# Performance work log

Measured on AMD Instinct MI355X. Metric: run time of the kernel, lower is better.

## Reference

```python
import jax, jax.numpy as jnp
import numpy as np

F_NODE, F_BOND, D, LAYERS = 133, 14, 256, 3
N_NODE, N_BOND, N_NB = 100000, 200000, 600000


def hardswish(x):
    return x * jnp.clip(x + 3.0, 0.0, 6.0) * (1.0 / 6.0)


def setup_inputs() -> dict:
    key = jax.random.key(0)
    ks = jax.random.split(key, 16)

    def xav(k, fan_in, fan_out):
        std = (2.0 / (fan_in + fan_out)) ** 0.5
        return (jax.random.normal(k, (fan_in, fan_out), jnp.float32) * std)

    inp = {
        "node": jax.random.normal(ks[0], (N_NODE, F_NODE), jnp.float32),
        "bond": jax.random.normal(ks[1], (N_BOND, F_BOND), jnp.float32),
        "connect": jax.random.randint(ks[2], (3, N_BOND), 0, N_NODE, jnp.int32),
        "bond_neighbour": jax.random.randint(ks[3], (2, N_NB), 0, N_BOND, jnp.int32),
        # learned parameters, stored as [in, out] (torch Linear transposed)
        "w_node": xav(ks[4], F_NODE, D), "b_node": jnp.zeros((D,), jnp.float32),
        "w_node_final": xav(ks[5], F_NODE + D, D), "b_node_final": jnp.zeros((D,), jnp.float32),
        "w_bond": xav(ks[6], F_NODE + F_BOND, D), "b_bond": jnp.zeros((D,), jnp.float32),
        "w_bond_final": xav(ks[7], F_NODE + F_BOND + D, D), "b_bond_final": jnp.zeros((D,), jnp.float32),
        "w_z": xav(ks[8], F_NODE + F_BOND + D, D), "b_z": jnp.zeros((D,), jnp.float32),
        "w_r": xav(ks[9], F_NODE + F_BOND + D, D), "b_r": jnp.zeros((D,), jnp.float32),
        "u": xav(ks[10], D, D),
        "w_m": xav(ks[11], F_NODE + F_BOND, D), "b_m": jnp.zeros((D,), jnp.float32),
        "w_n": xav(ks[12], F_NODE, D), "b_n": jnp.zeros((D,), jnp.float32),
        "u_n": xav(ks[13], 2 * D, D),
    }
    return inp


def reference(node, bond, connect, bond_neighbour,
              w_node, b_node, w_node_final, b_node_final,
              w_bond, b_bond, w_bond_final, b_bond_final,
              w_z, b_z, w_r, b_r, u, w_m, b_m, w_n, b_n, u_n):
    i_idx, j_idx = connect[0], connect[1]          # [E]; connect[2] (reverse) unused
    ij_idx, ki_idx = bond_neighbour[0], bond_neighbour[1]  # [E_nb]

    init_bond = jnp.concatenate([node[i_idx], bond], axis=-1)  # [E, f_node+f_bond]
    init_node = node                                           # [N, f_node]

    mess_bond = hardswish(init_bond @ w_bond + b_bond)  # [E, D]
    mess_node = hardswish(node @ w_node + b_node)       # [N, D]

    for _ in range(LAYERS):
        mess_ki = mess_bond[ki_idx]                                   # [E_nb, D]
        s_ij = jax.ops.segment_sum(mess_ki, ij_idx, num_segments=N_BOND)
        z_ij = jax.nn.sigmoid(jnp.concatenate([init_bond, s_ij], -1) @ w_z + b_z)
        r_ki = jax.nn.sigmoid(jnp.concatenate([init_bond[ij_idx], mess_ki], -1) @ w_r + b_r)
        r_ij = jax.ops.segment_sum(r_ki * mess_ki, ij_idx, num_segments=N_BOND)
        m_ij = jnp.tanh(init_bond @ w_m + b_m + r_ij @ u)
        mess_bond = (1.0 - z_ij) * s_ij + z_ij * m_ij                 # [E, D]
        aggr_node = jax.ops.segment_sum(mess_bond, j_idx, num_segments=N_NODE)
        mess_node = hardswish(init_node @ w_n + b_n
                              + jnp.concatenate([mess_node, aggr_node], -1) @ u_n)

    mess_bond = hardswish(jnp.concatenate([init_bond, mess_bond], -1) @ w_bond_final + b_bond_final)
    mess_node = hardswish(jnp.concatenate([init_node, mess_node], -1) @ w_node_final + b_node_final)
    # dropout is identity in eval mode
    return mess_node, mess_bond
```

## Files before the change

### kernel.cpp

```cpp
#include <hip/hip_runtime.h>
#include <hip/hip_bf16.h>

#define NN 100000
#define NE 200000
#define NB 600000
#define FN 133
#define FB 14
#define FIB 147
#define DD 256
#define NEPAD (196 * 1024)
#define NNPAD (98 * 1024)

typedef __hip_bfloat16 bf16;
typedef __attribute__((ext_vector_type(8))) short short8;
typedef __attribute__((ext_vector_type(4))) float f32x4;

__device__ __forceinline__ float hswish(float x) {
    float c = fminf(fmaxf(x + 3.f, 0.f), 6.f);
    return x * c * (1.f / 6.f);
}
__device__ __forceinline__ float sigmoidf(float x) {
    return 1.f / (1.f + __expf(-x));
}
__device__ __forceinline__ float tanh_fast(float x) {
    return 1.f - 2.f / (1.f + __expf(2.f * x));
}
__device__ __forceinline__ float bf2f(unsigned short u) {
    union { unsigned int i; float f; } c; c.i = (unsigned int)u << 16; return c.f;
}
__device__ __forceinline__ unsigned short f2bf(float v) {
    bf16 b = __float2bfloat16(v);
    unsigned short u; __builtin_memcpy(&u, &b, 2); return u;
}
__device__ __forceinline__ void unp8(short8 v, float* f) {
    #pragma unroll
    for (int j = 0; j < 8; j++) {
        short s = v[j]; unsigned short u; __builtin_memcpy(&u, &s, 2);
        f[j] = bf2f(u);
    }
}
__device__ __forceinline__ uint4 pk8(const float* f) {
    uint4 v;
    v.x = f2bf(f[0]) | ((unsigned)f2bf(f[1]) << 16);
    v.y = f2bf(f[2]) | ((unsigned)f2bf(f[3]) << 16);
    v.z = f2bf(f[4]) | ((unsigned)f2bf(f[5]) << 16);
    v.w = f2bf(f[6]) | ((unsigned)f2bf(f[7]) << 16);
    return v;
}

__global__ __launch_bounds__(256) void fill_kernel(float* __restrict__ p, float v, long n4) {
    long i = (long)blockIdx.x * 256 + threadIdx.x;
    long st = (long)gridDim.x * 256;
    float4 z = {v, v, v, v};
    for (; i < n4; i += st) ((float4*)p)[i] = z;
}

__global__ __launch_bounds__(256) void build_ib_bf(
    const float* __restrict__ node, const float* __restrict__ bond,
    const int* __restrict__ i_idx, bf16* __restrict__ IB)
{
    int t = blockIdx.x * 256 + threadIdx.x;
    int row = t >> 6;
    if (row >= NE) return;
    int lane = t & 63;
    if (lane >= 40) return;
    int src = i_idx[row];
    int c = lane * 4;
    unsigned short us[4];
    #pragma unroll
    for (int j = 0; j < 4; j++) {
        int k = c + j;
        float v = 0.f;
        if (k < FN)       v = node[(size_t)src * FN + k];
        else if (k < FIB) v = bond[(size_t)row * FB + (k - FN)];
        us[j] = f2bf(v);
    }
    ushort4 o = {us[0], us[1], us[2], us[3]};
    *(ushort4*)((unsigned short*)IB + (size_t)row * 160 + c) = o;
}

__global__ __launch_bounds__(256) void zero2_kernel(int* __restrict__ offE, int* __restrict__ offN)
{
    int i = blockIdx.x * 256 + threadIdx.x;
    if (i < NEPAD) offE[i] = 0;
    else if (i < NEPAD + NNPAD) offN[i - NEPAD] = 0;
}

__global__ __launch_bounds__(256) void count2_kernel(
    const int* __restrict__ ij, const int* __restrict__ jidx,
    int* __restrict__ offE, int* __restrict__ offN)
{
    int i = blockIdx.x * 256 + threadIdx.x;
    if (i < NB) atomicAdd(&offE[ij[i]], 1);
    else if (i < NB + NE) atomicAdd(&offN[jidx[i - NB]], 1);
}

__global__ __launch_bounds__(256) void scan_block2(
    int* __restrict__ offE, int* __restrict__ offN,
    int* __restrict__ bsumE, int* __restrict__ bsumN)
{
    __shared__ int lds[256];
    int* data; int* bs; int bb;
    if ((int)blockIdx.x < 196) { data = offE; bs = bsumE; bb = blockIdx.x; }
    else                       { data = offN; bs = bsumN; bb = blockIdx.x - 196; }
    int base = bb * 1024 + threadIdx.x * 4;
    int c0 = data[base], c1 = data[base + 1], c2 = data[base + 2], c3 = data[base + 3];
    int t = c0 + c1 + c2 + c3;
    lds[threadIdx.x] = t;
    __syncthreads();
    int x = t;
    for (int off = 1; off < 256; off <<= 1) {
        int y = (threadIdx.x >= off) ? lds[threadIdx.x - off] : 0;
        __syncthreads();
        x += y; lds[threadIdx.x] = x;
        __syncthreads();
    }
    int excl = x - t;
    data[base] = excl; data[base + 1] = excl + c0;
    data[base + 2] = excl + c0 + c1; data[base + 3] = excl + c0 + c1 + c2;
    if (threadIdx.x == 255) bs[bb] = x;
}

__global__ __launch_bounds__(256) void scan_bsum2(int* __restrict__ bsumE, int* __restrict__ bsumN)
{
    __shared__ int lds[256];
    int* bs = blockIdx.x ? bsumN : bsumE;
    int n = blockIdx.x ? 98 : 196;
    int t = (threadIdx.x < n) ? bs[threadIdx.x] : 0;
    lds[threadIdx.x] = t;
    __syncthreads();
    int x = t;
    for (int off = 1; off < 256; off <<= 1) {
        int y = (threadIdx.x >= off) ? lds[threadIdx.x - off] : 0;
        __syncthreads();
        x += y; lds[threadIdx.x] = x;
        __syncthreads();
    }
    if (threadIdx.x < n) bs[threadIdx.x] = x - t;
}

__global__ __launch_bounds__(256) void scan_add_copy2(
    int* __restrict__ offE, int* __restrict__ offN,
    const int* __restrict__ bsumE, const int* __restrict__ bsumN,
    int* __restrict__ curE, int* __restrict__ curN)
{
    int i = blockIdx.x * 256 + threadIdx.x;
    if (i < NEPAD) {
        int v = offE[i] + bsumE[i >> 10];
        offE[i] = v; curE[i] = v;
    } else if (i < NEPAD + NNPAD) {
        int j = i - NEPAD;
        int v = offN[j] + bsumN[j >> 10];
        offN[j] = v; curN[j] = v;
    }
}

__global__ __launch_bounds__(256) void lists2_kernel(
    const int* __restrict__ ij, const int* __restrict__ ki, const int* __restrict__ jidx,
    int* __restrict__ curE, int* __restrict__ curN,
    int* __restrict__ nbLst, int* __restrict__ agLst)
{
    int i = blockIdx.x * 256 + threadIdx.x;
    if (i < NB) { int p = atomicAdd(&curE[ij[i]], 1); nbLst[p] = ki[i]; }
    else if (i < NB + NE) {
        int e = i - NB;
        int p = atomicAdd(&curN[jidx[e]], 1); agLst[p] = e;
    }
}

__global__ __launch_bounds__(256) void pack_all(
    const float* __restrict__ w_r, const float* __restrict__ w_z,
    const float* __restrict__ w_bond, const float* __restrict__ w_m,
    const float* __restrict__ w_node, const float* __restrict__ w_n,
    const float* __restrict__ u_, const float* __restrict__ u_n,
    const float* __restrict__ w_bf, const float* __restrict__ w_nf,
    bf16* __restrict__ wt)
{
    int idx = blockIdx.x * 256 + threadIdx.x;
    if (idx >= 786432) return;
    float v = 0.f;
    if (idx < 245760) {
        int r = idx / 40960;
        int loc = idx - r * 40960;
        int n = loc / 160, k = loc % 160;
        const float* W = (r == 0) ? w_r : (r == 1) ? w_z : (r == 2) ? w_bond
                       : (r == 3) ? w_m : (r == 4) ? w_node : w_n;
        int K1 = (r < 4) ? FIB : FN;
        if (k < K1) v = W[(size_t)k * DD + n];
    } else if (idx < 442368) {
        int r = (idx - 245760) / 65536;
        int loc = (idx - 245760) - r * 65536;
        int n = loc / 256, k = loc % 256;
        const float* W = (r == 0) ? (w_r + (size_t)FIB * DD)
                       : (r == 1) ? (w_z + (size_t)FIB * DD) : u_;
        v = W[(size_t)k * DD + n];
    } else if (idx < 573440) {
        int loc = idx - 442368;
        int n = loc / 512, k = loc % 512;
        v = u_n[(size_t)k * DD + n];
    } else {
        int r = (idx - 573440) / 106496;
        int loc = (idx - 573440) - r * 106496;
        int n = loc / 416, k = loc % 416;
        const float* W = r ? w_nf : w_bf;
        int K1 = r ? FN : FIB;
        if (k < K1)        v = W[(size_t)k * DD + n];
        else if (k >= 160) v = W[(size_t)(K1 + k - 160) * DD + n];
    }
    wt[idx] = __float2bfloat16(v);
}

__global__ __launch_bounds__(256) void seg_sr_kernel(
    const bf16* __restrict__ MB, const bf16* __restrict__ TR,
    const bf16* __restrict__ PR, const int* __restrict__ off,
    const int* __restrict__ lst,
    bf16* __restrict__ S, bf16* __restrict__ R)
{
    int sid = blockIdx.x * 4 + (threadIdx.x >> 6);
    if (sid >= NE) return;
    int lane = threadIdx.x & 63;
    ushort4 up = *(const ushort4*)((const unsigned short*)PR + (size_t)sid * DD + lane * 4);
    float p0 = bf2f(up.x), p1 = bf2f(up.y), p2 = bf2f(up.z), p3 = bf2f(up.w);
    int b = off[sid], e = off[sid + 1];
    float s0 = 0, s1 = 0, s2 = 0, s3 = 0;
    float r0 = 0, r1 = 0, r2 = 0, r3 = 0;
    for (int t = b; t < e; t++) {
        int src = lst[t];
        ushort4 um = *(const ushort4*)((const unsigned short*)MB + (size_t)src * DD + lane * 4);
        ushort4 ut = *(const ushort4*)((const unsigned short*)TR + (size_t)src * DD + lane * 4);
        float m0 = bf2f(um.x), m1 = bf2f(um.y), m2 = bf2f(um.z), m3 = bf2f(um.w);
        s0 += m0; s1 += m1; s2 += m2; s3 += m3;
        r0 += sigmoidf(p0 + bf2f(ut.x)) * m0;
        r1 += sigmoidf(p1 + bf2f(ut.y)) * m1;
        r2 += sigmoidf(p2 + bf2f(ut.z)) * m2;
        r3 += sigmoidf(p3 + bf2f(ut.w)) * m3;
    }
    ushort4 os = {f2bf(s0), f2bf(s1), f2bf(s2), f2bf(s3)};
    ushort4 orr = {f2bf(r0), f2bf(r1), f2bf(r2), f2bf(r3)};
    *(ushort4*)((unsigned short*)S + (size_t)sid * DD + lane * 4) = os;
    *(ushort4*)((unsigned short*)R + (size_t)sid * DD + lane * 4) = orr;
}

__global__ __launch_bounds__(512) void blend2(
    const bf16* __restrict__ S, const bf16* __restrict__ R,
    const bf16* __restrict__ WTz2, const bf16* __restrict__ WTu,
    const bf16* __restrict__ PZ, const bf16* __restrict__ PM,
    bf16* __restrict__ MB)
{
    __shared__ __align__(16) unsigned short As[128 * 72];
    __shared__ __align__(16) unsigned short Bs[128 * 72];
    const int tid = threadIdx.x;
    const int row0 = blockIdx.x * 128, col0 = blockIdx.y * 128;
    const int lane = tid & 63, w = tid >> 6;
    const int wr = w >> 1, wc = w & 1;
    const int fr = lane & 15, ko = (lane >> 4) * 8;

    f32x4 acc1[2][4] = {};
    f32x4 acc2[2][4] = {};

    #pragma unroll
    for (int ph = 0; ph < 2; ph++) {
        const bf16* A = (ph == 0) ? S : R;
        const bf16* W = (ph == 0) ? WTz2 : WTu;
        for (int k0 = 0; k0 < DD; k0 += 64) {
            {
                int mloc = tid >> 2, kq = (tid & 3) * 16;
                int mg = row0 + mloc;
                uint4 va = {0, 0, 0, 0}, va2 = {0, 0, 0, 0};
                if (mg < NE) {
                    va  = *(const uint4*)((const unsigned short*)A + (size_t)mg * DD + k0 + kq);
                    va2 = *(const uint4*)((const unsigned short*)A + (size_t)mg * DD + k0 + kq + 8);
                }
                uint4 vb  = *(const uint4*)((const unsigned short*)W + (size_t)(col0 + mloc) * DD + k0 + kq);
                uint4 vb2 = *(const uint4*)((const unsigned short*)W + (size_t)(col0 + mloc) * DD + k0 + kq + 8);
                *(uint4*)&As[mloc * 72 + kq] = va;
                *(uint4*)&As[mloc * 72 + kq + 8] = va2;
                *(uint4*)&Bs[mloc * 72 + kq] = vb;
                *(uint4*)&Bs[mloc * 72 + kq + 8] = vb2;
            }
            __syncthreads();
            #pragma unroll
            for (int kk = 0; kk < 64; kk += 32) {
                short8 af[2], bf8[4];
                #pragma unroll
                for (int mf = 0; mf < 2; mf++)
                    af[mf] = *(const short8*)&As[(wr * 32 + mf * 16 + fr) * 72 + kk + ko];
                #pragma unroll
                for (int nf = 0; nf < 4; nf++)
                    bf8[nf] = *(const short8*)&Bs[(wc * 64 + nf * 16 + fr) * 72 + kk + ko];
                #pragma unroll
                for (int mf = 0; mf < 2; mf++)
                    #pragma unroll
                    for (int nf = 0; nf < 4; nf++) {
                        if (ph == 0)
                            acc1[mf][nf] = __builtin_amdgcn_mfma_f32_16x16x32_bf16(af[mf], bf8[nf], acc1[mf][nf], 0, 0, 0);
                        else
                            acc2[mf][nf] = __builtin_amdgcn_mfma_f32_16x16x32_bf16(af[mf], bf8[nf], acc2[mf][nf], 0, 0, 0);
                    }
            }
            __syncthreads();
        }
    }

    #pragma unroll
    for (int mf = 0; mf < 2; mf++) {
        #pragma unroll
        for (int i = 0; i < 4; i++) {
            int mloc = wr * 32 + mf * 16 + (lane >> 4) * 4 + i;
            int gm = row0 + mloc;
            if (gm >= NE) continue;
            #pragma unroll
            for (int nf = 0; nf < 4; nf++) {
                int gc = col0 + wc * 64 + nf * 16 + fr;
                size_t idx = (size_t)gm * DD + gc;
                float z  = sigmoidf(acc1[mf][nf][i] + __bfloat162float(PZ[idx]));
                float mm = tanh_fast(acc2[mf][nf][i] + __bfloat162float(PM[idx]));
                float s  = __bfloat162float(S[idx]);
                MB[idx] = __float2bfloat16((1.f - z) * s + z * mm);
            }
        }
    }
}

__global__ __launch_bounds__(512) void pairk(
    int trblocks,
    const bf16* __restrict__ MBn, const bf16* __restrict__ WTr2,
    bf16* __restrict__ TRo,
    const bf16* __restrict__ MN, const int* __restrict__ offN,
    const int* __restrict__ agLst, const bf16* __restrict__ WTnu,
    const bf16* __restrict__ PN, bf16* __restrict__ MNout)
{
    __shared__ __align__(16) unsigned short As[128 * 40];
    __shared__ __align__(16) unsigned short Bs[256 * 40];
    const int tid = threadIdx.x, lane = tid & 63, w = tid >> 6;
    const int fr = lane & 15, ko = (lane >> 4) * 8;
    const int mloc = tid >> 2, kq = (tid & 3) * 8;

    if ((int)blockIdx.x < trblocks) {
        const int row0 = blockIdx.x * 128;
        const int wr = w >> 2, wc = w & 3;
        const int mg = row0 + mloc;
        f32x4 acc[4][4] = {};
        for (int k0 = 0; k0 < 256; k0 += 32) {
            uint4 v = {0, 0, 0, 0};
            if (mg < NE)
                v = *(const uint4*)((const unsigned short*)MBn + (size_t)mg * DD + k0 + kq);
            *(uint4*)&As[mloc * 40 + kq] = v;
            #pragma unroll
            for (int it = 0; it < 2; ++it) {
                int nloc = (tid >> 2) + it * 128;
                *(uint4*)&Bs[nloc * 40 + kq] =
                    *(const uint4*)((const unsigned short*)WTr2 + (size_t)nloc * DD + k0 + kq);
            }
            __syncthreads();
            short8 af[4], bw[4];
            #pragma unroll
            for (int mf = 0; mf < 4; mf++)
                af[mf] = *(const short8*)&As[(wr * 64 + mf * 16 + fr) * 40 + ko];
            #pragma unroll
            for (int nf = 0; nf < 4; nf++)
                bw[nf] = *(const short8*)&Bs[(wc * 64 + nf * 16 + fr) * 40 + ko];
            #pragma unroll
            for (int mf = 0; mf < 4; mf++)
                #pragma unroll
                for (int nf = 0; nf < 4; nf++)
                    acc[mf][nf] = __builtin_amdgcn_mfma_f32_16x16x32_bf16(af[mf], bw[nf], acc[mf][nf], 0, 0, 0);
            __syncthreads();
        }
        #pragma unroll
        for (int mf = 0; mf < 4; mf++)
            #pragma unroll
            for (int i = 0; i < 4; i++) {
                int ml = wr * 64 + mf * 16 + (lane >> 4) * 4 + i;
                int gm = row0 + ml;
                if (gm >= NE) continue;
                #pragma unroll
                for (int nf = 0; nf < 4; nf++) {
                    int gc = wc * 64 + nf * 16 + fr;
                    TRo[(size_t)gm * DD + gc] = __float2bfloat16(acc[mf][nf][i]);
                }
            }
    } else {
        const int bx = blockIdx.x - trblocks;
        const int row0 = bx * 128;
        const int wr = w >> 2, wc = w & 3;
        const int mg = row0 + mloc;
        int eb = 0, ee = 0;
        if (mg < NN) { eb = offN[mg]; ee = offN[mg + 1]; }
        f32x4 acc[4][4] = {};
        for (int k0 = 0; k0 < 512; k0 += 32) {
            const int kg = k0 + kq;
            uint4 v = {0, 0, 0, 0};
            if (mg < NN) {
                if (kg < 256) {
                    v = *(const uint4*)((const unsigned short*)MN + (size_t)mg * DD + kg);
                } else {
                    const int kk = kg - 256;
                    float a[8] = {0, 0, 0, 0, 0, 0, 0, 0};
                    for (int t = eb; t < ee; t++) {
                        int src = agLst[t];
                        float m8[8];
                        unp8(*(const short8*)((const unsigned short*)MBn + (size_t)src * DD + kk), m8);
                        #pragma unroll
                        for (int j = 0; j < 8; j++) a[j] += m8[j];
                    }
                    v = pk8(a);
                }
            }
            *(uint4*)&As[mloc * 40 + kq] = v;
            #pragma unroll
            for (int it = 0; it < 2; ++it) {
                int nloc = (tid >> 2) + it * 128;
                *(uint4*)&Bs[nloc * 40 + kq] =
                    *(const uint4*)((const unsigned short*)WTnu + (size_t)nloc * 512 + k0 + kq);
            }
            __syncthreads();
            short8 af[4], bw[4];
            #pragma unroll
            for (int mf = 0; mf < 4; mf++)
                af[mf] = *(const short8*)&As[(wr * 64 + mf * 16 + fr) * 40 + ko];
            #pragma unroll
            for (int nf = 0; nf < 4; nf++)
                bw[nf] = *(const short8*)&Bs[(wc * 64 + nf * 16 + fr) * 40 + ko];
            #pragma unroll
            for (int mf = 0; mf < 4; mf++)
                #pragma unroll
                for (int nf = 0; nf < 4; nf++)
                    acc[mf][nf] = __builtin_amdgcn_mfma_f32_16x16x32_bf16(af[mf], bw[nf], acc[mf][nf], 0, 0, 0);
            __syncthreads();
        }
        #pragma unroll
        for (int mf = 0; mf < 4; mf++)
            #pragma unroll
            for (int i = 0; i < 4; i++) {
                int ml = wr * 64 + mf * 16 + (lane >> 4) * 4 + i;
                int gm = row0 + ml;
                if (gm >= NN) continue;
                #pragma unroll
                for (int nf = 0; nf < 4; nf++) {
                    int gc = wc * 64 + nf * 16 + fr;
                    size_t idx = (size_t)gm * DD + gc;
                    MNout[idx] = __float2bfloat16(
                        hswish(acc[mf][nf][i] + __bfloat162float(PN[idx])));
                }
            }
    }
}

template <int BN, int NT, int DUAL, int EPB>
__device__ __forceinline__ void bg_body(
    const void* __restrict__ A1, int a1stride, int a1kw, int a1real, int a1f32,
    const void* __restrict__ A2, int a2stride, int a2kw, int a2real, int a2f32,
    const bf16* __restrict__ WT1, const bf16* __restrict__ WT2, int KT,
    const float* __restrict__ bias1, const float* __restrict__ bias2,
    void* __restrict__ out1, void* __restrict__ out2, int M,
    int row0, int col0,
    unsigned short* As, unsigned short* Bs, unsigned short* Bs2)
{
    constexpr int BM = 128;
    constexpr int nWc = BN / 64;
    constexpr int nWr = (NT / 64) / nWc;
    constexpr int MSPAN = BM / nWr;
    constexpr int MFR = MSPAN / 16;
    const int tid = threadIdx.x;
    const int lane = tid & 63, w = tid >> 6;
    const int wr = w / nWc, wc = w % nWc;
    const int fr = lane & 15, ko = (lane >> 4) * 8;

    f32x4 acc[MFR][4] = {};
    f32x4 acc2[DUAL ? MFR : 1][DUAL ? 4 : 1] = {};

    for (int k0 = 0; k0 < KT; k0 += 32) {
        #pragma unroll
        for (int it = 0; it < BM * 4 / NT; ++it) {
            int mloc = (tid >> 2) + it * (NT / 4);
            int mg = row0 + mloc;
            bool mok = (mg < M);
            int kq = (tid & 3) * 8;
            int kg = k0 + kq;
            const void* p; int stride, real, isf; int kk;
            if (kg < a1kw) { p = A1; stride = a1stride; real = a1real; isf = a1f32; kk = kg; }
            else           { p = A2; stride = a2stride; real = a2real; isf = a2f32; kk = kg - a1kw; }
            uint4 v = {0, 0, 0, 0};
            if (mok) {
                if (!isf) {
                    v = *(const uint4*)((const bf16*)p + (size_t)mg * stride + kk);
                } else {
                    const float* fp = (const float*)p + (size_t)mg * stride;
                    unsigned short us[8];
                    #pragma unroll
                    for (int j = 0; j < 8; j++)
                        us[j] = (kk + j < real) ? f2bf(fp[kk + j]) : (unsigned short)0;
                    v.x = us[0] | ((unsigned)us[1] << 16);
                    v.y = us[2] | ((unsigned)us[3] << 16);
                    v.z = us[4] | ((unsigned)us[5] << 16);
                    v.w = us[6] | ((unsigned)us[7] << 16);
                }
            }
            *(uint4*)&As[mloc * 40 + kq] = v;
        }
        #pragma unroll
        for (int it = 0; it < BN * 4 / NT; ++it) {
            int nloc = (tid >> 2) + it * (NT / 4);
            int kq = (tid & 3) * 8;
            *(uint4*)&Bs[nloc * 40 + kq] =
                *(const uint4*)&WT1[(size_t)(col0 + nloc) * KT + k0 + kq];
            if (DUAL)
                *(uint4*)&Bs2[nloc * 40 + kq] =
                    *(const uint4*)&WT2[(size_t)(col0 + nloc) * KT + k0 + kq];
        }
        __syncthreads();
        short8 a1f[MFR], b1f[4], b2f[DUAL ? 4 : 1];
        #pragma unroll
        for (int mf = 0; mf < MFR; mf++)
            a1f[mf] = *(const short8*)&As[(wr * MSPAN + mf * 16 + fr) * 40 + ko];
        #pragma unroll
        for (int nf = 0; nf < 4; nf++) {
            b1f[nf] = *(const short8*)&Bs[(wc * 64 + nf * 16 + fr) * 40 + ko];
            if (DUAL)
                b2f[nf] = *(const short8*)&Bs2[(wc * 64 + nf * 16 + fr) * 40 + ko];
        }
        #pragma unroll
        for (int mf = 0; mf < MFR; mf++)
            #pragma unroll
            for (int nf = 0; nf < 4; nf++) {
                acc[mf][nf] = __builtin_amdgcn_mfma_f32_16x16x32_bf16(a1f[mf], b1f[nf], acc[mf][nf], 0, 0, 0);
                if (DUAL)
                    acc2[mf][nf] = __builtin_amdgcn_mfma_f32_16x16x32_bf16(a1f[mf], b2f[nf], acc2[mf][nf], 0, 0, 0);
            }
        __syncthreads();
    }

    #pragma unroll
    for (int mf = 0; mf < MFR; mf++) {
        #pragma unroll
        for (int i = 0; i < 4; i++) {
            int mloc = wr * MSPAN + mf * 16 + (lane >> 4) * 4 + i;
            int gm = row0 + mloc;
            if (gm >= M) continue;
            #pragma unroll
            for (int nf = 0; nf < 4; nf++) {
                int gc = col0 + wc * 64 + nf * 16 + fr;
                size_t idx = (size_t)gm * DD + gc;
                float v = acc[mf][nf][i];
                if (EPB == 0) {
                    if (bias1) v += bias1[gc];
                    ((bf16*)out1)[idx] = __float2bfloat16(v);
                } else if (EPB == 2) {
                    ((bf16*)out1)[idx] = __float2bfloat16(hswish(v + bias1[gc]));
                    ((bf16*)out2)[idx] = __float2bfloat16(acc2[mf][nf][i] + bias2[gc]);
                } else if (EPB == 3) {
                    ((bf16*)out1)[idx] = __float2bfloat16(v + bias1[gc]);
                    ((bf16*)out2)[idx] = __float2bfloat16(acc2[mf][nf][i] + bias2[gc]);
                } else {
                    ((float*)out1)[idx] = hswish(v + bias1[gc]);
                }
            }
        }
    }
}

__device__ __forceinline__ void bg64_body(
    const void* __restrict__ A1, int a1stride, int a1kw, int a1real, int a1f32,
    const void* __restrict__ A2, int a2stride, int a2kw, int a2real, int a2f32,
    const bf16* __restrict__ WT1, int KT, const float* __restrict__ bias1,
    float* __restrict__ out1, int M, int row0,
    unsigned short* As, unsigned short* Bs)
{
    const int tid = threadIdx.x;
    const int lane = tid & 63, w = tid >> 6;
    const int wr = w >> 2, wc = w & 3;
    const int fr = lane & 15, ko = (lane >> 4) * 8;

    f32x4 acc[2][4] = {};

    for (int k0 = 0; k0 < KT; k0 += 32) {
        if (tid < 256) {
            int mloc = tid >> 2, kq = (tid & 3) * 8;
            int mg = row0 + mloc;
            int kg = k0 + kq;
            const void* p; int stride, real, isf; int kk;
            if (kg < a1kw) { p = A1; stride = a1stride; real = a1real; isf = a1f32; kk = kg; }
            else           { p = A2; stride = a2stride; real = a2real; isf = a2f32; kk = kg - a1kw; }
            uint4 v = {0, 0, 0, 0};
            if (mg < M) {
                if (!isf) {
                    v = *(const uint4*)((const bf16*)p + (size_t)mg * stride + kk);
                } else {
                    const float* fp = (const float*)p + (size_t)mg * stride;
                    unsigned short us[8];
                    #pragma unroll
                    for (int j = 0; j < 8; j++)
                        us[j] = (kk + j < real) ? f2bf(fp[kk + j]) : (unsigned short)0;
                    v.x = us[0] | ((unsigned)us[1] << 16);
                    v.y = us[2] | ((unsigned)us[3] << 16);
                    v.z = us[4] | ((unsigned)us[5] << 16);
                    v.w = us[6] | ((unsigned)us[7] << 16);
                }
            }
            *(uint4*)&As[mloc * 40 + kq] = v;
        }
        {
            int kq = (tid & 3) * 8;
            #pragma unroll
            for (int it = 0; it < 2; ++it) {
                int nloc = (tid >> 2) + it * 128;
                *(uint4*)&Bs[nloc * 40 + kq] =
                    *(const uint4*)&WT1[(size_t)nloc * KT + k0 + kq];
            }
        }
        __syncthreads();
        short8 af[2], bw[4];
        #pragma unroll
        for (int mf = 0; mf < 2; mf++)
            af[mf] = *(const short8*)&As[(wr * 32 + mf * 16 + fr) * 40 + ko];
        #pragma unroll
        for (int nf = 0; nf < 4; nf++)
            bw[nf] = *(const short8*)&Bs[(wc * 64 + nf * 16 + fr) * 40 + ko];
        #pragma unroll
        for (int mf = 0; mf < 2; mf++)
            #pragma unroll
            for (int nf = 0; nf < 4; nf++)
                acc[mf][nf] = __builtin_amdgcn_mfma_f32_16x16x32_bf16(af[mf], bw[nf], acc[mf][nf], 0, 0, 0);
        __syncthreads();
    }

    #pragma unroll
    for (int mf = 0; mf < 2; mf++) {
        #pragma unroll
        for (int i = 0; i < 4; i++) {
            int mloc = wr * 32 + mf * 16 + (lane >> 4) * 4 + i;
            int gm = row0 + mloc;
            if (gm >= M) continue;
            #pragma unroll
            for (int nf = 0; nf < 4; nf++) {
                int gc = wc * 64 + nf * 16 + fr;
                out1[(size_t)gm * DD + gc] = hswish(acc[mf][nf][i] + bias1[gc]);
            }
        }
    }
}

__global__ __launch_bounds__(512) void pre_pair1(
    const bf16* __restrict__ IBbf,
    const bf16* __restrict__ WTr, const bf16* __restrict__ WTz1,
    const float* __restrict__ b_r, const float* __restrict__ b_z,
    bf16* __restrict__ PR, bf16* __restrict__ PZ,
    const bf16* __restrict__ WTb, const bf16* __restrict__ WTm1,
    const float* __restrict__ b_bond, const float* __restrict__ b_m,
    bf16* __restrict__ MB, bf16* __restrict__ PM)
{
    __shared__ __align__(16) unsigned short As[128 * 40];
    __shared__ __align__(16) unsigned short Bs[128 * 40];
    __shared__ __align__(16) unsigned short Bs2[128 * 40];
    int b = blockIdx.x;
    if (b < 3126) {
        int bx = b % 1563, by = b / 1563;
        bg_body<128, 512, 1, 3>(IBbf, 160, 160, 160, 0, nullptr, 0, 0, 0, 0,
            WTr, WTz1, 160, b_r, b_z, PR, PZ, NE, bx * 128, by * 128, As, Bs, Bs2);
    } else {
        int b2 = b - 3126;
        int bx = b2 % 1563, by = b2 / 1563;
        bg_body<128, 512, 1, 2>(IBbf, 160, 160, 160, 0, nullptr, 0, 0, 0, 0,
            WTb, WTm1, 160, b_bond, b_m, MB, PM, NE, bx * 128, by * 128, As, Bs, Bs2);
    }
}

__global__ __launch_bounds__(512) void pre_pair2(
    const float* __restrict__ node,
    const bf16* __restrict__ WTn0, const bf16* __restrict__ WTn,
    const float* __restrict__ b_node, const float* __restrict__ b_n,
    bf16* __restrict__ MN, bf16* __restrict__ PN,
    const bf16* __restrict__ MB, const bf16* __restrict__ WTr2,
    bf16* __restrict__ TR)
{
    __shared__ __align__(16) unsigned short As[128 * 40];
    __shared__ __align__(16) unsigned short Bs[128 * 40];
    __shared__ __align__(16) unsigned short Bs2[128 * 40];
    int b = blockIdx.x;
    if (b < 1564) {
        int bx = b % 782, by = b / 782;
        bg_body<128, 512, 1, 2>(node, FN, 160, FN, 1, nullptr, 0, 0, 0, 0,
            WTn0, WTn, 160, b_node, b_n, MN, PN, NN, bx * 128, by * 128, As, Bs, Bs2);
    } else {
        int b2 = b - 1564;
        int bx = b2 % 1563, by = b2 / 1563;
        bg_body<128, 512, 0, 0>(MB, 256, 256, 256, 0, nullptr, 0, 0, 0, 0,
            WTr2, nullptr, 256, nullptr, nullptr, TR, nullptr, NE,
            bx * 128, by * 128, As, Bs, Bs2);
    }
}

__global__ __launch_bounds__(512) void final_pair64(
    const bf16* __restrict__ IBbf, const bf16* __restrict__ MB,
    const bf16* __restrict__ WTbf, const float* __restrict__ b_bf,
    float* __restrict__ out_bond,
    const float* __restrict__ node, const bf16* __restrict__ MNf,
    const bf16* __restrict__ WTnf, const float* __restrict__ b_nf,
    float* __restrict__ out_node)
{
    __shared__ __align__(16) unsigned short As[64 * 40];
    __shared__ __align__(16) unsigned short Bs[256 * 40];
    int b = blockIdx.x;
    if (b < 3125) {
        bg64_body(IBbf, 160, 160, 160, 0, MB, 256, 256, 256, 0,
                  WTbf, 416, b_bf, out_bond, NE, b * 64, As, Bs);
    } else {
        bg64_body(node, FN, 160, FN, 1, MNf, 256, 256, 256, 0,
                  WTnf, 416, b_nf, out_node, NN, (b - 3125) * 64, As, Bs);
    }
}

extern "C" void kernel_launch(void* const* d_in, const int* in_sizes, int n_in,
                              void* d_out, int out_size, void* d_ws, size_t ws_size,
                              hipStream_t stream)
{
    const float* node  = (const float*)d_in[0];
    const float* bond  = (const float*)d_in[1];
    const int* connect = (const int*)d_in[2];
    const int* bnb     = (const int*)d_in[3];
    const float* w_node       = (const float*)d_in[4];
    const float* b_node       = (const float*)d_in[5];
    const float* w_node_final = (const float*)d_in[6];
    const float* b_node_final = (const float*)d_in[7];
    const float* w_bond       = (const float*)d_in[8];
    const float* b_bond       = (const float*)d_in[9];
    const float* w_bond_final = (const float*)d_in[10];
    const float* b_bond_final = (const float*)d_in[11];
    const float* w_z = (const float*)d_in[12];
    const float* b_z = (const float*)d_in[13];
    const float* w_r = (const float*)d_in[14];
    const float* b_r = (const float*)d_in[15];
    const float* u_  = (const float*)d_in[16];
    const float* w_m = (const float*)d_in[17];
    const float* b_m = (const float*)d_in[18];
    const float* w_n = (const float*)d_in[19];
    const float* b_n = (const float*)d_in[20];
    const float* u_n = (const float*)d_in[21];

    const int* i_idx = connect;
    const int* j_idx = connect + NE;
    const int* ij    = bnb;
    const int* ki    = bnb + NB;

    const size_t EBH = (size_t)NE * DD * 2;
    const size_t B_WT = (size_t)786432 * 2;
    const size_t B_CSR = (size_t)NEPAD * 8 + (size_t)NB * 4
                       + (size_t)NNPAD * 8 + (size_t)NE * 4 + 2048;
    const size_t NEED = 5 * EBH + B_WT + B_CSR;

    float* out_node = (float*)d_out;
    float* out_bond = out_node + (size_t)NN * DD;

    if (ws_size < NEED) {
        fill_kernel<<<2048, 256, 0, stream>>>((float*)d_out, 1e6f, (long)out_size / 4);
        return;
    }

    char* base = (char*)d_ws;
    bf16* PR = (bf16*)base;                       base += EBH;
    bf16* MB = (bf16*)base;                       base += EBH;
    bf16* TR = (bf16*)base;                       base += EBH;
    bf16* PZ = (bf16*)base;                       base += EBH;
    bf16* PM = (bf16*)base;                       base += EBH;
    char* wt = base;                              base += B_WT;
    int* offE  = (int*)base;                      base += (size_t)NEPAD * 4;
    int* curE  = (int*)base;                      base += (size_t)NEPAD * 4;
    int* nbLst = (int*)base;                      base += (size_t)NB * 4;
    int* offN  = (int*)base;                      base += (size_t)NNPAD * 4;
    int* curN  = (int*)base;                      base += (size_t)NNPAD * 4;
    int* agLst = (int*)base;                      base += (size_t)NE * 4;
    int* bsumE = (int*)base;                      base += 1024;
    int* bsumN = (int*)base;

    bf16* IBbf = TR;
    bf16* MNf = PR;
    bf16* R = (bf16*)out_bond;
    bf16* S = R + (size_t)NE * DD;
    bf16* MN = (bf16*)out_node;
    bf16* PN = MN + (size_t)NN * DD;

    bf16* wtb = (bf16*)wt;
    bf16* WTr  = wtb + 0;
    bf16* WTz1 = wtb + 40960;
    bf16* WTb  = wtb + 81920;
    bf16* WTm1 = wtb + 122880;
    bf16* WTn0 = wtb + 163840;
    bf16* WTn  = wtb + 204800;
    bf16* WTr2 = wtb + 245760;
    bf16* WTz2 = wtb + 311296;
    bf16* WTu  = wtb + 376832;
    bf16* WTnu = wtb + 442368;
    bf16* WTbf = wtb + 573440;
    bf16* WTnf = wtb + 679936;

    pack_all<<<3072, 256, 0, stream>>>(w_r, w_z, w_bond, w_m, w_node, w_n,
                                       u_, u_n, w_bond_final, w_node_final, wtb);

    zero2_kernel<<<(NEPAD + NNPAD + 255) / 256, 256, 0, stream>>>(offE, offN);
    count2_kernel<<<(NB + NE + 255) / 256, 256, 0, stream>>>(ij, j_idx, offE, offN);
    scan_block2<<<294, 256, 0, stream>>>(offE, offN, bsumE, bsumN);
    scan_bsum2<<<2, 256, 0, stream>>>(bsumE, bsumN);
    scan_add_copy2<<<(NEPAD + NNPAD + 255) / 256, 256, 0, stream>>>(
        offE, offN, bsumE, bsumN, curE, curN);
    lists2_kernel<<<(NB + NE + 255) / 256, 256, 0, stream>>>(ij, ki, j_idx,
                                                             curE, curN, nbLst, agLst);

    int blkIB = NE * 64 / 256;
    dim3 gB2(1563, 2);

    build_ib_bf<<<blkIB, 256, 0, stream>>>(node, bond, i_idx, IBbf);
    pre_pair1<<<6252, 512, 0, stream>>>(IBbf, WTr, WTz1, b_r, b_z, PR, PZ,
                                        WTb, WTm1, b_bond, b_m, MB, PM);
    pre_pair2<<<4690, 512, 0, stream>>>(node, WTn0, WTn, b_node, b_n, MN, PN,
                                        MB, WTr2, TR);

    for (int l = 0; l < 3; l++) {
        seg_sr_kernel<<<(NE + 3) / 4, 256, 0, stream>>>(MB, TR, PR, offE, nbLst, S, R);
        blend2<<<gB2, 512, 0, stream>>>(S, R, WTz2, WTu, PZ, PM, MB);
        int trb = (l < 2) ? 1563 : 0;
        bf16* mnout = (l == 2) ? MNf : MN;
        pairk<<<trb + 782, 512, 0, stream>>>(trb, MB, WTr2, TR,
                                             MN, offN, agLst, WTnu, PN, mnout);
    }

    build_ib_bf<<<blkIB, 256, 0, stream>>>(node, bond, i_idx, IBbf);
    final_pair64<<<4688, 512, 0, stream>>>(IBbf, MB, WTbf, b_bond_final, out_bond,
                                           node, MNf, WTnf, b_node_final, out_node);
}
```

Before: 2.425 ms.

## Interleave bond messages and TR projections in one row-major buffer for gather locality

```diff
diff --git a/kernel.cpp b/kernel.cpp
--- a/kernel.cpp
+++ b/kernel.cpp
@@ -8,6 +8,7 @@
 #define FB 14
 #define FIB 147
 #define DD 256
+#define MTS 512
 #define NEPAD (196 * 1024)
 #define NNPAD (98 * 1024)
 
@@ -211,9 +212,8 @@
 }
 
 __global__ __launch_bounds__(256) void seg_sr_kernel(
-    const bf16* __restrict__ MB, const bf16* __restrict__ TR,
-    const bf16* __restrict__ PR, const int* __restrict__ off,
-    const int* __restrict__ lst,
+    const bf16* __restrict__ MBT, const bf16* __restrict__ PR,
+    const int* __restrict__ off, const int* __restrict__ lst,
     bf16* __restrict__ S, bf16* __restrict__ R)
 {
     int sid = blockIdx.x * 4 + (threadIdx.x >> 6);
@@ -226,8 +226,9 @@
     float r0 = 0, r1 = 0, r2 = 0, r3 = 0;
     for (int t = b; t < e; t++) {
         int src = lst[t];
-        ushort4 um = *(const ushort4*)((const unsigned short*)MB + (size_t)src * DD + lane * 4);
-        ushort4 ut = *(const ushort4*)((const unsigned short*)TR + (size_t)src * DD + lane * 4);
+        const unsigned short* row = (const unsigned short*)MBT + (size_t)src * MTS;
+        ushort4 um = *(const ushort4*)(row + lane * 4);
+        ushort4 ut = *(const ushort4*)(row + 256 + lane * 4);
         float m0 = bf2f(um.x), m1 = bf2f(um.y), m2 = bf2f(um.z), m3 = bf2f(um.w);
         s0 += m0; s1 += m1; s2 += m2; s3 += m3;
         r0 += sigmoidf(p0 + bf2f(ut.x)) * m0;
@@ -245,7 +246,7 @@
     const bf16* __restrict__ S, const bf16* __restrict__ R,
     const bf16* __restrict__ WTz2, const bf16* __restrict__ WTu,
     const bf16* __restrict__ PZ, const bf16* __restrict__ PM,
-    bf16* __restrict__ MB)
+    bf16* __restrict__ MBT)
 {
     __shared__ __align__(16) unsigned short As[128 * 72];
     __shared__ __align__(16) unsigned short Bs[128 * 72];
@@ -316,7 +317,7 @@
                 float z  = sigmoidf(acc1[mf][nf][i] + __bfloat162float(PZ[idx]));
                 float mm = tanh_fast(acc2[mf][nf][i] + __bfloat162float(PM[idx]));
                 float s  = __bfloat162float(S[idx]);
-                MB[idx] = __float2bfloat16((1.f - z) * s + z * mm);
+                MBT[(size_t)gm * MTS + gc] = __float2bfloat16((1.f - z) * s + z * mm);
             }
         }
     }
@@ -324,11 +325,11 @@
 
 __global__ __launch_bounds__(512) void pairk(
     int trblocks,
-    const bf16* __restrict__ MBn, const bf16* __restrict__ WTr2,
-    bf16* __restrict__ TRo,
+    const bf16* __restrict__ MBT, const bf16* __restrict__ WTr2,
     const bf16* __restrict__ MN, const int* __restrict__ offN,
     const int* __restrict__ agLst, const bf16* __restrict__ WTnu,
-    const bf16* __restrict__ PN, bf16* __restrict__ MNout)
+    const bf16* __restrict__ PN, bf16* __restrict__ MNout,
+    bf16* __restrict__ MBTw)
 {
     __shared__ __align__(16) unsigned short As[128 * 40];
     __shared__ __align__(16) unsigned short Bs[256 * 40];
@@ -344,7 +345,7 @@
         for (int k0 = 0; k0 < 256; k0 += 32) {
             uint4 v = {0, 0, 0, 0};
             if (mg < NE)
-                v = *(const uint4*)((const unsigned short*)MBn + (size_t)mg * DD + k0 + kq);
+                v = *(const uint4*)((const unsigned short*)MBT + (size_t)mg * MTS + k0 + kq);
             *(uint4*)&As[mloc * 40 + kq] = v;
             #pragma unroll
             for (int it = 0; it < 2; ++it) {
@@ -377,7 +378,7 @@
                 #pragma unroll
                 for (int nf = 0; nf < 4; nf++) {
                     int gc = wc * 64 + nf * 16 + fr;
-                    TRo[(size_t)gm * DD + gc] = __float2bfloat16(acc[mf][nf][i]);
+                    MBTw[(size_t)gm * MTS + 256 + gc] = __float2bfloat16(acc[mf][nf][i]);
                 }
             }
     } else {
@@ -400,7 +401,7 @@
                     for (int t = eb; t < ee; t++) {
                         int src = agLst[t];
                         float m8[8];
-                        unp8(*(const short8*)((const unsigned short*)MBn + (size_t)src * DD + kk), m8);
+                        unp8(*(const short8*)((const unsigned short*)MBT + (size_t)src * MTS + kk), m8);
                         #pragma unroll
                         for (int j = 0; j < 8; j++) a[j] += m8[j];
                     }
@@ -454,7 +455,7 @@
     const bf16* __restrict__ WT1, const bf16* __restrict__ WT2, int KT,
     const float* __restrict__ bias1, const float* __restrict__ bias2,
     void* __restrict__ out1, void* __restrict__ out2, int M,
-    int row0, int col0,
+    int row0, int col0, int os1, int os2,
     unsigned short* As, unsigned short* Bs, unsigned short* Bs2)
 {
     constexpr int BM = 128;
@@ -541,19 +542,20 @@
             #pragma unroll
             for (int nf = 0; nf < 4; nf++) {
                 int gc = col0 + wc * 64 + nf * 16 + fr;
-                size_t idx = (size_t)gm * DD + gc;
+                size_t i1 = (size_t)gm * os1 + gc;
+                size_t i2 = (size_t)gm * os2 + gc;
                 float v = acc[mf][nf][i];
                 if (EPB == 0) {
                     if (bias1) v += bias1[gc];
-                    ((bf16*)out1)[idx] = __float2bfloat16(v);
+                    ((bf16*)out1)[i1] = __float2bfloat16(v);
                 } else if (EPB == 2) {
-                    ((bf16*)out1)[idx] = __float2bfloat16(hswish(v + bias1[gc]));
-                    ((bf16*)out2)[idx] = __float2bfloat16(acc2[mf][nf][i] + bias2[gc]);
+                    ((bf16*)out1)[i1] = __float2bfloat16(hswish(v + bias1[gc]));
+                    ((bf16*)out2)[i2] = __float2bfloat16(acc2[mf][nf][i] + bias2[gc]);
                 } else if (EPB == 3) {
-                    ((bf16*)out1)[idx] = __float2bfloat16(v + bias1[gc]);
-                    ((bf16*)out2)[idx] = __float2bfloat16(acc2[mf][nf][i] + bias2[gc]);
+                    ((bf16*)out1)[i1] = __float2bfloat16(v + bias1[gc]);
+                    ((bf16*)out2)[i2] = __float2bfloat16(acc2[mf][nf][i] + bias2[gc]);
                 } else {
-                    ((float*)out1)[idx] = hswish(v + bias1[gc]);
+                    ((float*)out1)[i1] = hswish(v + bias1[gc]);
                 }
             }
         }
@@ -648,7 +650,7 @@
     bf16* __restrict__ PR, bf16* __restrict__ PZ,
     const bf16* __restrict__ WTb, const bf16* __restrict__ WTm1,
     const float* __restrict__ b_bond, const float* __restrict__ b_m,
-    bf16* __restrict__ MB, bf16* __restrict__ PM)
+    bf16* __restrict__ MBT, bf16* __restrict__ PM)
 {
     __shared__ __align__(16) unsigned short As[128 * 40];
     __shared__ __align__(16) unsigned short Bs[128 * 40];
@@ -657,12 +659,12 @@
     if (b < 3126) {
         int bx = b % 1563, by = b / 1563;
         bg_body<128, 512, 1, 3>(IBbf, 160, 160, 160, 0, nullptr, 0, 0, 0, 0,
-            WTr, WTz1, 160, b_r, b_z, PR, PZ, NE, bx * 128, by * 128, As, Bs, Bs2);
+            WTr, WTz1, 160, b_r, b_z, PR, PZ, NE, bx * 128, by * 128, DD, DD, As, Bs, Bs2);
     } else {
         int b2 = b - 3126;
         int bx = b2 % 1563, by = b2 / 1563;
         bg_body<128, 512, 1, 2>(IBbf, 160, 160, 160, 0, nullptr, 0, 0, 0, 0,
-            WTb, WTm1, 160, b_bond, b_m, MB, PM, NE, bx * 128, by * 128, As, Bs, Bs2);
+            WTb, WTm1, 160, b_bond, b_m, MBT, PM, NE, bx * 128, by * 128, MTS, DD, As, Bs, Bs2);
     }
 }
 
@@ -671,8 +673,8 @@
     const bf16* __restrict__ WTn0, const bf16* __restrict__ WTn,
     const float* __restrict__ b_node, const float* __restrict__ b_n,
     bf16* __restrict__ MN, bf16* __restrict__ PN,
-    const bf16* __restrict__ MB, const bf16* __restrict__ WTr2,
-    bf16* __restrict__ TR)
+    const bf16* __restrict__ MBT, const bf16* __restrict__ WTr2,
+    bf16* __restrict__ TRout)
 {
     __shared__ __align__(16) unsigned short As[128 * 40];
     __shared__ __align__(16) unsigned short Bs[128 * 40];
@@ -681,18 +683,18 @@
     if (b < 1564) {
         int bx = b % 782, by = b / 782;
         bg_body<128, 512, 1, 2>(node, FN, 160, FN, 1, nullptr, 0, 0, 0, 0,
-            WTn0, WTn, 160, b_node, b_n, MN, PN, NN, bx * 128, by * 128, As, Bs, Bs2);
+            WTn0, WTn, 160, b_node, b_n, MN, PN, NN, bx * 128, by * 128, DD, DD, As, Bs, Bs2);
     } else {
         int b2 = b - 1564;
         int bx = b2 % 1563, by = b2 / 1563;
-        bg_body<128, 512, 0, 0>(MB, 256, 256, 256, 0, nullptr, 0, 0, 0, 0,
-            WTr2, nullptr, 256, nullptr, nullptr, TR, nullptr, NE,
-            bx * 128, by * 128, As, Bs, Bs2);
+        bg_body<128, 512, 0, 0>(MBT, MTS, 256, 256, 0, nullptr, 0, 0, 0, 0,
+            WTr2, nullptr, 256, nullptr, nullptr, TRout, nullptr, NE,
+            bx * 128, by * 128, MTS, MTS, As, Bs, Bs2);
     }
 }
 
 __global__ __launch_bounds__(512) void final_pair64(
-    const bf16* __restrict__ IBbf, const bf16* __restrict__ MB,
+    const bf16* __restrict__ IBbf, const bf16* __restrict__ MBT,
     const bf16* __restrict__ WTbf, const float* __restrict__ b_bf,
     float* __restrict__ out_bond,
     const float* __restrict__ node, const bf16* __restrict__ MNf,
@@ -703,7 +705,7 @@
     __shared__ __align__(16) unsigned short Bs[256 * 40];
     int b = blockIdx.x;
     if (b < 3125) {
-        bg64_body(IBbf, 160, 160, 160, 0, MB, 256, 256, 256, 0,
+        bg64_body(IBbf, 160, 160, 160, 0, MBT, MTS, 256, 256, 0,
                   WTbf, 416, b_bf, out_bond, NE, b * 64, As, Bs);
     } else {
         bg64_body(node, FN, 160, FN, 1, MNf, 256, 256, 256, 0,
@@ -758,11 +760,10 @@
     }
 
     char* base = (char*)d_ws;
-    bf16* PR = (bf16*)base;                       base += EBH;
-    bf16* MB = (bf16*)base;                       base += EBH;
-    bf16* TR = (bf16*)base;                       base += EBH;
-    bf16* PZ = (bf16*)base;                       base += EBH;
-    bf16* PM = (bf16*)base;                       base += EBH;
+    bf16* PR  = (bf16*)base;                      base += EBH;
+    bf16* MBT = (bf16*)base;                      base += 2 * EBH;
+    bf16* PZ  = (bf16*)base;                      base += EBH;
+    bf16* PM  = (bf16*)base;                      base += EBH;
     char* wt = base;                              base += B_WT;
     int* offE  = (int*)base;                      base += (size_t)NEPAD * 4;
     int* curE  = (int*)base;                      base += (size_t)NEPAD * 4;
@@ -773,10 +774,11 @@
     int* bsumE = (int*)base;                      base += 1024;
     int* bsumN = (int*)base;
 
-    bf16* IBbf = TR;
-    bf16* MNf = PR;
     bf16* R = (bf16*)out_bond;
     bf16* S = R + (size_t)NE * DD;
+    bf16* IBpre = R;
+    bf16* IBfin = PZ;
+    bf16* MNf = PR;
     bf16* MN = (bf16*)out_node;
     bf16* PN = MN + (size_t)NN * DD;
 
@@ -809,22 +811,22 @@
     int blkIB = NE * 64 / 256;
     dim3 gB2(1563, 2);
 
-    build_ib_bf<<<blkIB, 256, 0, stream>>>(node, bond, i_idx, IBbf);
-    pre_pair1<<<6252, 512, 0, stream>>>(IBbf, WTr, WTz1, b_r, b_z, PR, PZ,
-                                        WTb, WTm1, b_bond, b_m, MB, PM);
+    build_ib_bf<<<blkIB, 256, 0, stream>>>(node, bond, i_idx, IBpre);
+    pre_pair1<<<6252, 512, 0, stream>>>(IBpre, WTr, WTz1, b_r, b_z, PR, PZ,
+                                        WTb, WTm1, b_bond, b_m, MBT, PM);
     pre_pair2<<<4690, 512, 0, stream>>>(node, WTn0, WTn, b_node, b_n, MN, PN,
-                                        MB, WTr2, TR);
+                                        MBT, WTr2, MBT + 256);
 
     for (int l = 0; l < 3; l++) {
-        seg_sr_kernel<<<(NE + 3) / 4, 256, 0, stream>>>(MB, TR, PR, offE, nbLst, S, R);
-        blend2<<<gB2, 512, 0, stream>>>(S, R, WTz2, WTu, PZ, PM, MB);
+        seg_sr_kernel<<<(NE + 3) / 4, 256, 0, stream>>>(MBT, PR, offE, nbLst, S, R);
+        blend2<<<gB2, 512, 0, stream>>>(S, R, WTz2, WTu, PZ, PM, MBT);
         int trb = (l < 2) ? 1563 : 0;
         bf16* mnout = (l == 2) ? MNf : MN;
-        pairk<<<trb + 782, 512, 0, stream>>>(trb, MB, WTr2, TR,
-                                             MN, offN, agLst, WTnu, PN, mnout);
-    }
-
-    build_ib_bf<<<blkIB, 256, 0, stream>>>(node, bond, i_idx, IBbf);
-    final_pair64<<<4688, 512, 0, stream>>>(IBbf, MB, WTbf, b_bond_final, out_bond,
+        pairk<<<trb + 782, 512, 0, stream>>>(trb, MBT, WTr2,
+                                             MN, offN, agLst, WTnu, PN, mnout, MBT);
+    }
+
+    build_ib_bf<<<blkIB, 256, 0, stream>>>(node, bond, i_idx, IBfin);
+    final_pair64<<<4688, 512, 0, stream>>>(IBfin, MBT, WTbf, b_bond_final, out_bond,
                                            node, MNf, WTnf, b_node_final, out_node);
 }
```

Measured after the change: 2.437 ms. Within noise of the previous version (+0.5%).
